# Optimization experiments

Hardware: AMD Instinct MI355X
Metric: run time of the kernel (lower is better)

Reference implementation:

```python
import jax, jax.numpy as jnp
import numpy as np

B, T, C = 4, 2048, 1024
H, DH = 16, 64  # num_heads, head_size; H*DH == C


def setup_inputs() -> dict:
    key = jax.random.key(0)
    ks = jax.random.split(key, 6)
    s = C ** -0.5  # mimic nn.Linear default init scale roughly
    x = jax.random.normal(ks[0], (B, T, C), dtype=jnp.float32)
    Wq = jax.random.normal(ks[1], (H, C, DH), dtype=jnp.float32) * s
    Wk = jax.random.normal(ks[2], (H, C, DH), dtype=jnp.float32) * s
    Wv = jax.random.normal(ks[3], (H, C, DH), dtype=jnp.float32) * s
    Wo = jax.random.normal(ks[4], (C, C), dtype=jnp.float32) * s
    bo = jax.random.normal(ks[5], (C,), dtype=jnp.float32) * s
    return {"x": x, "Wq": Wq, "Wk": Wk, "Wv": Wv, "Wo": Wo, "bo": bo}


def reference(x, Wq, Wk, Wv, Wo, bo):
    # per-head projections (no bias, as in nanoGPT Head)
    q = jnp.einsum('btc,hcd->bhtd', x, Wq)
    k = jnp.einsum('btc,hcd->bhtd', x, Wk)
    v = jnp.einsum('btc,hcd->bhtd', x, Wv)
    scale = DH ** -0.5
    scores = jnp.einsum('bhtd,bhsd->bhts', q, k) * scale  # [B,H,T,T]
    causal = jnp.tril(jnp.ones((T, T), dtype=bool))
    scores = jnp.where(causal, scores, jnp.float32(-jnp.inf))
    attn = jax.nn.softmax(scores, axis=-1)
    out = jnp.einsum('bhts,bhsd->bhtd', attn, v)  # [B,H,T,DH]
    out = out.transpose(0, 2, 1, 3).reshape(B, T, C)  # concat heads
    return out @ Wo.T + bo  # output projection (dropout=0.0 -> identity)
```

## Files before the change

### kernel.cpp

```cpp
#include <hip/hip_runtime.h>
#include <hip/hip_bf16.h>

constexpr int kB = 4, kT = 2048, kC = 1024, kH = 16, kD = 64;

typedef __attribute__((ext_vector_type(8))) short bf16x8;
typedef __attribute__((ext_vector_type(4))) short bf16x4;
typedef __attribute__((ext_vector_type(4))) float f32x4;
typedef unsigned short u16;

__device__ inline u16 f2b(float f) {
    __bf16 h = (__bf16)f;
    return __builtin_bit_cast(u16, h);
}

__device__ __forceinline__ void gl_lds16(const u16* g, u16* l) {
    __builtin_amdgcn_global_load_lds(
        (__attribute__((address_space(1))) const void*)g,
        (__attribute__((address_space(3))) void*)l, 16, 0, 0);
}

__global__ __launch_bounds__(256) void prep_kernel(const float* __restrict__ xf,
                                                   u16* __restrict__ xb,
                                                   const float* __restrict__ Wq,
                                                   const float* __restrict__ Wk,
                                                   const float* __restrict__ Wv,
                                                   u16* __restrict__ Wt) {
    __shared__ u16 tile[64][66];
    if (blockIdx.x < 8192) {
        int i = (blockIdx.x * 256 + threadIdx.x) * 4;
        float4 v = *(const float4*)(xf + i);
        ushort4 o;
        o.x = f2b(v.x); o.y = f2b(v.y); o.z = f2b(v.z); o.w = f2b(v.w);
        *(ushort4*)(xb + i) = o;
        return;
    }
    int blk = blockIdx.x - 8192;
    int ct = blk & 15;
    int h  = (blk >> 4) & 15;
    int which = blk >> 8;
    const float* W = (which == 0) ? Wq : (which == 1) ? Wk : Wv;
    const float* src = W + ((size_t)h * kC + ct * 64) * kD;
    int tid = threadIdx.x;
    int dr = (tid & 15) * 4;
    int cr = tid >> 4;
    #pragma unroll
    for (int pass = 0; pass < 4; pass++) {
        int c = pass * 16 + cr;
        float4 v = *(const float4*)(src + (size_t)c * kD + dr);
        tile[c][dr + 0] = f2b(v.x);
        tile[c][dr + 1] = f2b(v.y);
        tile[c][dr + 2] = f2b(v.z);
        tile[c][dr + 3] = f2b(v.w);
    }
    __syncthreads();
    u16* dst = Wt + ((size_t)(which * kH + h) * kD) * kC + ct * 64;
    int c4 = (tid & 15) * 4;
    int d0 = tid >> 4;
    #pragma unroll
    for (int pass = 0; pass < 4; pass++) {
        int d = pass * 16 + d0;
        ushort4 pk;
        pk.x = tile[c4 + 0][d];
        pk.y = tile[c4 + 1][d];
        pk.z = tile[c4 + 2][d];
        pk.w = tile[c4 + 3][d];
        *(ushort4*)(dst + (size_t)d * kC + c4) = pk;
    }
}

__global__ __launch_bounds__(256) void qkv_kernel(const u16* __restrict__ x,
                                                  const u16* __restrict__ Wt,
                                                  u16* __restrict__ q,
                                                  u16* __restrict__ k,
                                                  u16* __restrict__ vT) {
    __shared__ u16 Ash[128 * 32];
    __shared__ u16 Bsh[128 * 32];
    const int tid = threadIdx.x;
    const int lane = tid & 63;
    const int w = tid >> 6;
    const int mblk = blockIdx.x & 63;
    const int nblk = blockIdx.x >> 6;
    const int m0 = mblk * 128, n0 = nblk * 128;
    const int wm = (w >> 1) * 64, wn = (w & 1) * 64;
    const int col = lane & 15, quad = lane >> 4;

    const int rowa = tid >> 2;
    const int kc = (tid & 3) * 8;
    const u16* gA = x + (size_t)(m0 + rowa) * kC + kc;
    const u16* gB = Wt + (size_t)(n0 + rowa) * kC + kc;
    u16* lA = Ash + tid * 8;
    u16* lB = Bsh + tid * 8;

    f32x4 z = {0.f, 0.f, 0.f, 0.f};
    f32x4 acc[4][4];
    #pragma unroll
    for (int mi = 0; mi < 4; mi++)
        #pragma unroll
        for (int ni = 0; ni < 4; ni++) acc[mi][ni] = z;

    for (int k0 = 0; k0 < kC; k0 += 32) {
        __syncthreads();
        gl_lds16(gA + k0, lA);
        gl_lds16(gA + (size_t)64 * kC + k0, lA + 64 * 32);
        gl_lds16(gB + k0, lB);
        gl_lds16(gB + (size_t)64 * kC + k0, lB + 64 * 32);
        __syncthreads();
        bf16x8 a[4], b[4];
        #pragma unroll
        for (int mi = 0; mi < 4; mi++)
            a[mi] = *(const bf16x8*)&Ash[(wm + mi * 16 + col) * 32 + quad * 8];
        #pragma unroll
        for (int ni = 0; ni < 4; ni++)
            b[ni] = *(const bf16x8*)&Bsh[(wn + ni * 16 + col) * 32 + quad * 8];
        #pragma unroll
        for (int mi = 0; mi < 4; mi++)
            #pragma unroll
            for (int ni = 0; ni < 4; ni++)
                acc[mi][ni] = __builtin_amdgcn_mfma_f32_16x16x32_bf16(a[mi], b[ni], acc[mi][ni], 0, 0, 0);
    }

    const int nq = n0 + wn;
    const int which = nq >> 10;
    const int h = (nq & 1023) >> 6;
    const int mq = m0 + wm;
    const int b_ = mq >> 11;
    const int tq = mq & 2047;
    if (which < 2) {
        const float qs = (which == 0) ? 0.1803368801111204f : 1.0f;
        u16* base = ((which == 0) ? q : k) + ((size_t)(b_ * kH + h) * kT) * kD;
        #pragma unroll
        for (int mi = 0; mi < 4; mi++)
            #pragma unroll
            for (int ni = 0; ni < 4; ni++)
                #pragma unroll
                for (int r = 0; r < 4; r++) {
                    int t = tq + mi * 16 + quad * 4 + r;
                    base[(size_t)t * kD + ni * 16 + col] = f2b(acc[mi][ni][r] * qs);
                }
    } else {
        u16* base = vT + ((size_t)(b_ * kH + h) * kD) * kT;
        #pragma unroll
        for (int mi = 0; mi < 4; mi++)
            #pragma unroll
            for (int ni = 0; ni < 4; ni++) {
                int d = ni * 16 + col;
                int t = tq + mi * 16 + quad * 4;
                ushort4 pk;
                pk.x = f2b(acc[mi][ni][0]);
                pk.y = f2b(acc[mi][ni][1]);
                pk.z = f2b(acc[mi][ni][2]);
                pk.w = f2b(acc[mi][ni][3]);
                *(ushort4*)(base + (size_t)d * kT + t) = pk;
            }
    }
}

__device__ __forceinline__ void attn_step(const bf16x8 (&ka)[2][2],
                                          const bf16x4 (&va)[2][4],
                                          const bf16x8 (&qa)[2][2],
                                          f32x4 (&o)[2][4],
                                          float (&l_)[2],
                                          bool needmask,
                                          int s0, int t0, int col, int quad) {
    f32x4 z = {0.f, 0.f, 0.f, 0.f};
    f32x4 st[2][2];
    #pragma unroll
    for (int si = 0; si < 2; si++)
        #pragma unroll
        for (int mi = 0; mi < 2; mi++) {
            f32x4 a = __builtin_amdgcn_mfma_f32_16x16x32_bf16(ka[si][0], qa[mi][0], z, 0, 0, 0);
            st[si][mi] = __builtin_amdgcn_mfma_f32_16x16x32_bf16(ka[si][1], qa[mi][1], a, 0, 0, 0);
        }
    bf16x4 pb[2][2];
    #pragma unroll
    for (int mi = 0; mi < 2; mi++)
        #pragma unroll
        for (int si = 0; si < 2; si++) {
            bf16x4 pk;
            #pragma unroll
            for (int r = 0; r < 4; r++) {
                float p = __builtin_amdgcn_exp2f(st[si][mi][r]);
                if (needmask) {
                    int sg = s0 + si * 16 + quad * 4 + r;
                    int tg = t0 + mi * 16 + col;
                    if (sg > tg) p = 0.f;
                }
                l_[mi] += p;
                pk[r] = (short)f2b(p);
            }
            pb[mi][si] = pk;
        }
    #pragma unroll
    for (int si = 0; si < 2; si++)
        #pragma unroll
        for (int dt = 0; dt < 4; dt++)
            #pragma unroll
            for (int mi = 0; mi < 2; mi++)
                o[mi][dt] = __builtin_amdgcn_mfma_f32_16x16x16bf16_1k(va[si][dt], pb[mi][si], o[mi][dt], 0, 0, 0);
}

__global__ __launch_bounds__(256) void attn_kernel(const u16* __restrict__ q,
                                                   const u16* __restrict__ kmat,
                                                   const u16* __restrict__ vT,
                                                   u16* __restrict__ att,
                                                   const float* __restrict__ Wo,
                                                   u16* __restrict__ Wob) {
    __shared__ u16 shmem[4][2][4096];
    if (blockIdx.x >= 512) {
        int i = ((blockIdx.x - 512) * 256 + threadIdx.x) * 4;
        float4 v = *(const float4*)(Wo + i);
        ushort4 o;
        o.x = f2b(v.x); o.y = f2b(v.y); o.z = f2b(v.z); o.w = f2b(v.w);
        *(ushort4*)(Wob + i) = o;
        return;
    }
    const int tid = threadIdx.x;
    const int lane = tid & 63;
    const int w = tid >> 6;
    const int bh = blockIdx.x & 63;
    const int p8 = blockIdx.x >> 6;
    const int p = p8 * 4 + w;
    const int t0a = p * 32;
    const int t0b = (63 - p) * 32;
    const int Lw = 63 - p8 * 4 - w;
    const int col = lane & 15, quad = lane >> 4;

    const u16* qbase = q + (size_t)bh * kT * kD;
    const u16* kbase = kmat + (size_t)bh * kT * kD;
    const u16* vbase = vT + (size_t)bh * kD * kT;

    const u16* gK0 = kbase + (size_t)(lane >> 3) * kD + (((lane & 7) ^ (lane >> 3)) * 8);
    const u16* gV0 = vbase + (size_t)(lane >> 2) * kT + (((lane & 3) ^ ((lane >> 3) & 3)) * 8);

    bf16x8 qa[2][2][2];
    #pragma unroll
    for (int tile = 0; tile < 2; tile++) {
        int t0 = tile ? t0b : t0a;
        #pragma unroll
        for (int mi = 0; mi < 2; mi++)
            #pragma unroll
            for (int c2 = 0; c2 < 2; c2++)
                qa[tile][mi][c2] = *(const bf16x8*)(qbase + (size_t)(t0 + mi * 16 + col) * kD + c2 * 32 + quad * 8);
    }
    asm volatile("s_waitcnt vmcnt(0)" ::: "memory");

    f32x4 z = {0.f, 0.f, 0.f, 0.f};
    f32x4 oA[2][4], oB[2][4];
    #pragma unroll
    for (int mi = 0; mi < 2; mi++)
        #pragma unroll
        for (int dt = 0; dt < 4; dt++) { oA[mi][dt] = z; oB[mi][dt] = z; }
    float lA[2] = {0.f, 0.f}, lB[2] = {0.f, 0.f};

    auto stage = [&](int buf, int tile) {
        u16* Kd = &shmem[w][buf][0] + lane * 8;
        u16* Vd = &shmem[w][buf][2048] + lane * 8;
        const u16* gk = gK0 + (size_t)(tile * 32) * kD;
        const u16* gv = gV0 + tile * 32;
        #pragma unroll
        for (int i = 0; i < 4; i++) {
            gl_lds16(gk + (size_t)(i * 8) * kD, Kd + i * 512);
            gl_lds16(gv + (size_t)(i * 16) * kT, Vd + i * 512);
        }
    };

    stage(0, 0);
    if (Lw >= 1) stage(1, 1);
    for (int j = 0; j <= Lw; j++) {
        if (j < Lw) { asm volatile("s_waitcnt vmcnt(8)" ::: "memory"); }
        else        { asm volatile("s_waitcnt vmcnt(0)" ::: "memory"); }
        const int buf = j & 1;
        const u16* Kb = &shmem[w][buf][0];
        const u16* Vb = Kb + 2048;
        bf16x8 ka[2][2];
        #pragma unroll
        for (int si = 0; si < 2; si++) {
            int row = si * 16 + col;
            #pragma unroll
            for (int c2 = 0; c2 < 2; c2++)
                ka[si][c2] = *(const bf16x8*)&Kb[row * 64 + (((c2 * 4 + quad) ^ (row & 7)) * 8)];
        }
        bf16x4 va[2][4];
        #pragma unroll
        for (int si = 0; si < 2; si++)
            #pragma unroll
            for (int dt = 0; dt < 4; dt++) {
                int row = dt * 16 + col;
                int sb = si * 2 + (quad >> 1);
                va[si][dt] = *(const bf16x4*)&Vb[row * 32 + ((sb ^ ((row >> 1) & 3)) * 8) + (quad & 1) * 4];
            }
        asm volatile("s_waitcnt lgkmcnt(0)" ::: "memory");
        if (j + 2 <= Lw) stage(buf, j + 2);
        const int s0 = j * 32;
        attn_step(ka, va, qa[1], oB, lB, j == Lw, s0, t0b, col, quad);
        if (j <= p)
            attn_step(ka, va, qa[0], oA, lA, j == p, s0, t0a, col, quad);
    }

    #pragma unroll
    for (int mi = 0; mi < 2; mi++) {
        lA[mi] += __shfl_xor(lA[mi], 16, 64);
        lA[mi] += __shfl_xor(lA[mi], 32, 64);
        lB[mi] += __shfl_xor(lB[mi], 16, 64);
        lB[mi] += __shfl_xor(lB[mi], 32, 64);
    }

    const int b = bh / kH, hh = bh % kH;
    #pragma unroll
    for (int tile = 0; tile < 2; tile++) {
        int t0 = tile ? t0b : t0a;
        #pragma unroll
        for (int mi = 0; mi < 2; mi++) {
            float inv = 1.0f / (tile ? lB[mi] : lA[mi]);
            int t = t0 + mi * 16 + col;
            #pragma unroll
            for (int dt = 0; dt < 4; dt++) {
                f32x4 s = tile ? oB[mi][dt] : oA[mi][dt];
                ushort4 pk;
                pk.x = f2b(s[0] * inv);
                pk.y = f2b(s[1] * inv);
                pk.z = f2b(s[2] * inv);
                pk.w = f2b(s[3] * inv);
                *(ushort4*)(att + ((size_t)b * kT + t) * kC + hh * kD + dt * 16 + quad * 4) = pk;
            }
        }
    }
}

__global__ __launch_bounds__(256) void oproj_kernel(const u16* __restrict__ att,
                                                    const u16* __restrict__ Wo,
                                                    const float* __restrict__ bo,
                                                    float* __restrict__ out) {
    __shared__ u16 Ash[128 * 32];
    __shared__ u16 Bsh[128 * 32];
    const int tid = threadIdx.x;
    const int lane = tid & 63;
    const int w = tid >> 6;
    const int mblk = blockIdx.x & 63;
    const int nblk = blockIdx.x >> 6;
    const int m0 = mblk * 128, n0 = nblk * 128;
    const int wm = (w >> 1) * 64, wn = (w & 1) * 64;
    const int col = lane & 15, quad = lane >> 4;

    const int rowa = tid >> 2;
    const int kc = (tid & 3) * 8;
    const u16* gA = att + (size_t)(m0 + rowa) * kC + kc;
    const u16* gB = Wo + (size_t)(n0 + rowa) * kC + kc;
    u16* lA = Ash + tid * 8;
    u16* lB = Bsh + tid * 8;

    f32x4 z = {0.f, 0.f, 0.f, 0.f};
    f32x4 acc[4][4];
    #pragma unroll
    for (int mi = 0; mi < 4; mi++)
        #pragma unroll
        for (int ni = 0; ni < 4; ni++) acc[mi][ni] = z;

    for (int k0 = 0; k0 < kC; k0 += 32) {
        __syncthreads();
        gl_lds16(gA + k0, lA);
        gl_lds16(gA + (size_t)64 * kC + k0, lA + 64 * 32);
        gl_lds16(gB + k0, lB);
        gl_lds16(gB + (size_t)64 * kC + k0, lB + 64 * 32);
        __syncthreads();
        bf16x8 a[4], b[4];
        #pragma unroll
        for (int mi = 0; mi < 4; mi++)
            a[mi] = *(const bf16x8*)&Ash[(wm + mi * 16 + col) * 32 + quad * 8];
        #pragma unroll
        for (int ni = 0; ni < 4; ni++)
            b[ni] = *(const bf16x8*)&Bsh[(wn + ni * 16 + col) * 32 + quad * 8];
        #pragma unroll
        for (int mi = 0; mi < 4; mi++)
            #pragma unroll
            for (int ni = 0; ni < 4; ni++)
                acc[mi][ni] = __builtin_amdgcn_mfma_f32_16x16x32_bf16(a[mi], b[ni], acc[mi][ni], 0, 0, 0);
    }

    float bias[4];
    #pragma unroll
    for (int ni = 0; ni < 4; ni++) bias[ni] = bo[n0 + wn + ni * 16 + col];

    #pragma unroll
    for (int mi = 0; mi < 4; mi++)
        #pragma unroll
        for (int ni = 0; ni < 4; ni++)
            #pragma unroll
            for (int r = 0; r < 4; r++) {
                int m = m0 + wm + mi * 16 + quad * 4 + r;
                out[(size_t)m * kC + n0 + wn + ni * 16 + col] = acc[mi][ni][r] + bias[ni];
            }
}

extern "C" void kernel_launch(void* const* d_in, const int* in_sizes, int n_in,
                              void* d_out, int out_size, void* d_ws, size_t ws_size,
                              hipStream_t stream) {
    const float* x  = (const float*)d_in[0];
    const float* Wq = (const float*)d_in[1];
    const float* Wk = (const float*)d_in[2];
    const float* Wv = (const float*)d_in[3];
    const float* Wo = (const float*)d_in[4];
    const float* bo = (const float*)d_in[5];
    float* out = (float*)d_out;

    char* ws = (char*)d_ws;
    u16* Wt  = (u16*)ws;
    u16* xb  = Wt + (size_t)3 * kH * kD * kC;
    u16* qb  = xb + (size_t)kB * kT * kC;
    u16* kb  = qb + (size_t)kB * kH * kT * kD;
    u16* vTb = kb + (size_t)kB * kH * kT * kD;
    u16* att = xb;
    u16* Wob = Wt;

    prep_kernel<<<dim3(8192 + 768), dim3(256), 0, stream>>>(x, xb, Wq, Wk, Wv, Wt);
    qkv_kernel<<<dim3(1536), dim3(256), 0, stream>>>(xb, Wt, qb, kb, vTb);
    attn_kernel<<<dim3(512 + 1024), dim3(256), 0, stream>>>(qb, kb, vTb, att, Wo, Wob);
    oproj_kernel<<<dim3(512), dim3(256), 0, stream>>>(att, Wob, bo, out);
}
```

Baseline: 247.9 us.

## Rewrite QKV GEMM with 256x256 tiles, 4-stage LDS pipeline and swizzle

The QKV projection GEMM moves from 128x128 tiles with 256 threads and a single synchronous LDS buffer to 256x256 tiles with 512 threads. It uses a four-buffer global-to-LDS prefetch ring with explicit vmcnt waits, an XOR swizzle on LDS rows to avoid bank conflicts, and interleaved half-tile MFMA phases with s_setprio. The aim is to hide global load latency and raise data reuse per block. The cost is more registers, 128KB of LDS per block, and only 384 blocks, which may underfill the GPU.

```diff
diff --git a/kernel.cpp b/kernel.cpp
--- a/kernel.cpp
+++ b/kernel.cpp
@@ -68,55 +68,93 @@
     }
 }
 
-__global__ __launch_bounds__(256) void qkv_kernel(const u16* __restrict__ x,
-                                                  const u16* __restrict__ Wt,
-                                                  u16* __restrict__ q,
-                                                  u16* __restrict__ k,
-                                                  u16* __restrict__ vT) {
-    __shared__ u16 Ash[128 * 32];
-    __shared__ u16 Bsh[128 * 32];
+__global__ __launch_bounds__(512, 2) void qkv_kernel(const u16* __restrict__ x,
+                                                     const u16* __restrict__ Wt,
+                                                     u16* __restrict__ q,
+                                                     u16* __restrict__ k,
+                                                     u16* __restrict__ vT) {
+    __shared__ u16 lds[4][2][8192];
     const int tid = threadIdx.x;
     const int lane = tid & 63;
     const int w = tid >> 6;
-    const int mblk = blockIdx.x & 63;
-    const int nblk = blockIdx.x >> 6;
-    const int m0 = mblk * 128, n0 = nblk * 128;
-    const int wm = (w >> 1) * 64, wn = (w & 1) * 64;
+    const int mblk = blockIdx.x & 31;
+    const int nblk = blockIdx.x >> 5;
+    const int m0 = mblk * 256, n0 = nblk * 256;
+    const int wm = (w >> 2) * 128, wn = (w & 3) * 64;
     const int col = lane & 15, quad = lane >> 4;
 
-    const int rowa = tid >> 2;
-    const int kc = (tid & 3) * 8;
-    const u16* gA = x + (size_t)(m0 + rowa) * kC + kc;
-    const u16* gB = Wt + (size_t)(n0 + rowa) * kC + kc;
-    u16* lA = Ash + tid * 8;
-    u16* lB = Bsh + tid * 8;
+    const int r0 = tid >> 2, kp = tid & 3;
+    const int r1 = r0 + 128;
+    const u16* gA0 = x  + (size_t)(m0 + r0) * kC + ((kp ^ ((r0 >> 1) & 3)) * 8);
+    const u16* gA1 = x  + (size_t)(m0 + r1) * kC + ((kp ^ ((r1 >> 1) & 3)) * 8);
+    const u16* gB0 = Wt + (size_t)(n0 + r0) * kC + ((kp ^ ((r0 >> 1) & 3)) * 8);
+    const u16* gB1 = Wt + (size_t)(n0 + r1) * kC + ((kp ^ ((r1 >> 1) & 3)) * 8);
+
+    auto stageA = [&](int buf, int kt) {
+        gl_lds16(gA0 + kt * 32, &lds[buf][0][0] + tid * 8);
+        gl_lds16(gA1 + kt * 32, &lds[buf][0][0] + (512 + tid) * 8);
+    };
+    auto stageB = [&](int buf, int kt) {
+        gl_lds16(gB0 + kt * 32, &lds[buf][1][0] + tid * 8);
+        gl_lds16(gB1 + kt * 32, &lds[buf][1][0] + (512 + tid) * 8);
+    };
 
     f32x4 z = {0.f, 0.f, 0.f, 0.f};
-    f32x4 acc[4][4];
-    #pragma unroll
-    for (int mi = 0; mi < 4; mi++)
+    f32x4 acc[8][4];
+    #pragma unroll
+    for (int mi = 0; mi < 8; mi++)
         #pragma unroll
         for (int ni = 0; ni < 4; ni++) acc[mi][ni] = z;
 
-    for (int k0 = 0; k0 < kC; k0 += 32) {
-        __syncthreads();
-        gl_lds16(gA + k0, lA);
-        gl_lds16(gA + (size_t)64 * kC + k0, lA + 64 * 32);
-        gl_lds16(gB + k0, lB);
-        gl_lds16(gB + (size_t)64 * kC + k0, lB + 64 * 32);
-        __syncthreads();
-        bf16x8 a[4], b[4];
+    stageA(0, 0); stageB(0, 0);
+    stageA(1, 1); stageB(1, 1);
+    stageA(2, 2); stageB(2, 2);
+    asm volatile("s_waitcnt vmcnt(8)" ::: "memory");
+    __builtin_amdgcn_s_barrier();
+
+    for (int g = 0; g < 32; g++) {
+        const int buf = g & 3;
+        const int sb = (g + 3) & 3;
+        const bool dos = (g + 3) < 32;
+        bf16x8 b0[4], a0[4], a1[4];
+        #pragma unroll
+        for (int ni = 0; ni < 4; ni++) {
+            int row = wn + ni * 16 + col;
+            b0[ni] = *(const bf16x8*)&lds[buf][1][row * 32 + ((quad ^ ((row >> 1) & 3)) * 8)];
+        }
+        #pragma unroll
+        for (int mi = 0; mi < 4; mi++) {
+            int row = wm + mi * 16 + col;
+            a0[mi] = *(const bf16x8*)&lds[buf][0][row * 32 + ((quad ^ ((row >> 1) & 3)) * 8)];
+        }
+        if (dos) stageA(sb, g + 3);
+        __builtin_amdgcn_s_barrier();
+        __builtin_amdgcn_s_setprio(1);
         #pragma unroll
         for (int mi = 0; mi < 4; mi++)
-            a[mi] = *(const bf16x8*)&Ash[(wm + mi * 16 + col) * 32 + quad * 8];
-        #pragma unroll
-        for (int ni = 0; ni < 4; ni++)
-            b[ni] = *(const bf16x8*)&Bsh[(wn + ni * 16 + col) * 32 + quad * 8];
+            #pragma unroll
+            for (int ni = 0; ni < 4; ni++)
+                acc[mi][ni] = __builtin_amdgcn_mfma_f32_16x16x32_bf16(a0[mi], b0[ni], acc[mi][ni], 0, 0, 0);
+        __builtin_amdgcn_s_setprio(0);
+        __builtin_amdgcn_s_barrier();
+        #pragma unroll
+        for (int mi = 0; mi < 4; mi++) {
+            int row = wm + 64 + mi * 16 + col;
+            a1[mi] = *(const bf16x8*)&lds[buf][0][row * 32 + ((quad ^ ((row >> 1) & 3)) * 8)];
+        }
+        if (dos) stageB(sb, g + 3);
+        __builtin_amdgcn_s_barrier();
+        __builtin_amdgcn_s_setprio(1);
         #pragma unroll
         for (int mi = 0; mi < 4; mi++)
             #pragma unroll
             for (int ni = 0; ni < 4; ni++)
-                acc[mi][ni] = __builtin_amdgcn_mfma_f32_16x16x32_bf16(a[mi], b[ni], acc[mi][ni], 0, 0, 0);
+                acc[4 + mi][ni] = __builtin_amdgcn_mfma_f32_16x16x32_bf16(a1[mi], b0[ni], acc[4 + mi][ni], 0, 0, 0);
+        __builtin_amdgcn_s_setprio(0);
+        if (g < 29)       { asm volatile("s_waitcnt vmcnt(8)" ::: "memory"); }
+        else if (g == 29) { asm volatile("s_waitcnt vmcnt(4)" ::: "memory"); }
+        else if (g == 30) { asm volatile("s_waitcnt vmcnt(0)" ::: "memory"); }
+        __builtin_amdgcn_s_barrier();
     }
 
     const int nq = n0 + wn;
@@ -129,7 +167,7 @@
         const float qs = (which == 0) ? 0.1803368801111204f : 1.0f;
         u16* base = ((which == 0) ? q : k) + ((size_t)(b_ * kH + h) * kT) * kD;
         #pragma unroll
-        for (int mi = 0; mi < 4; mi++)
+        for (int mi = 0; mi < 8; mi++)
             #pragma unroll
             for (int ni = 0; ni < 4; ni++)
                 #pragma unroll
@@ -140,7 +178,7 @@
     } else {
         u16* base = vT + ((size_t)(b_ * kH + h) * kD) * kT;
         #pragma unroll
-        for (int mi = 0; mi < 4; mi++)
+        for (int mi = 0; mi < 8; mi++)
             #pragma unroll
             for (int ni = 0; ni < 4; ni++) {
                 int d = ni * 16 + col;
@@ -413,7 +451,7 @@
     u16* Wob = Wt;
 
     prep_kernel<<<dim3(8192 + 768), dim3(256), 0, stream>>>(x, xb, Wq, Wk, Wv, Wt);
-    qkv_kernel<<<dim3(1536), dim3(256), 0, stream>>>(xb, Wt, qb, kb, vTb);
+    qkv_kernel<<<dim3(384), dim3(512), 0, stream>>>(xb, Wt, qb, kb, vTb);
     attn_kernel<<<dim3(512 + 1024), dim3(256), 0, stream>>>(qb, kb, vTb, att, Wo, Wob);
     oproj_kernel<<<dim3(512), dim3(256), 0, stream>>>(att, Wob, bo, out);
 }
```

After: 250.7 us. Within noise of the previous version (+1.1%).

## Triple-buffer QKV GEMM LDS loads with swizzled layout and async waits

Applied to the files above, without the earlier changes.

Replaces the QKV projection GEMM's single-buffered LDS staging, which had two barriers per k-step, with a three-stage ring. Global-to-LDS loads for later k-tiles are issued while MFMA runs on the current tile, and manual vmcnt waits plus s_barrier control the handoff. It also XOR-swizzles the 8-element chunks within each 32-wide row to reduce LDS bank conflicts on the fragment reads. LDS use triples, and the hand-written waitcnt sequence is fragile: the compiler's own waits or a change in counts could break correctness.

```diff
diff --git a/kernel.cpp b/kernel.cpp
--- a/kernel.cpp
+++ b/kernel.cpp
@@ -73,8 +73,7 @@
                                                   u16* __restrict__ q,
                                                   u16* __restrict__ k,
                                                   u16* __restrict__ vT) {
-    __shared__ u16 Ash[128 * 32];
-    __shared__ u16 Bsh[128 * 32];
+    __shared__ u16 lds[3][2][4096];
     const int tid = threadIdx.x;
     const int lane = tid & 63;
     const int w = tid >> 6;
@@ -84,12 +83,19 @@
     const int wm = (w >> 1) * 64, wn = (w & 1) * 64;
     const int col = lane & 15, quad = lane >> 4;
 
-    const int rowa = tid >> 2;
-    const int kc = (tid & 3) * 8;
-    const u16* gA = x + (size_t)(m0 + rowa) * kC + kc;
-    const u16* gB = Wt + (size_t)(n0 + rowa) * kC + kc;
-    u16* lA = Ash + tid * 8;
-    u16* lB = Bsh + tid * 8;
+    const int r0 = tid >> 2, kp = tid & 3;
+    const int r1 = r0 + 64;
+    const u16* gA0 = x  + (size_t)(m0 + r0) * kC + ((kp ^ ((r0 >> 1) & 3)) * 8);
+    const u16* gA1 = x  + (size_t)(m0 + r1) * kC + ((kp ^ ((r1 >> 1) & 3)) * 8);
+    const u16* gB0 = Wt + (size_t)(n0 + r0) * kC + ((kp ^ ((r0 >> 1) & 3)) * 8);
+    const u16* gB1 = Wt + (size_t)(n0 + r1) * kC + ((kp ^ ((r1 >> 1) & 3)) * 8);
+
+    auto stage = [&](int buf, int kt) {
+        gl_lds16(gA0 + kt * 32, &lds[buf][0][0] + tid * 8);
+        gl_lds16(gA1 + kt * 32, &lds[buf][0][0] + (256 + tid) * 8);
+        gl_lds16(gB0 + kt * 32, &lds[buf][1][0] + tid * 8);
+        gl_lds16(gB1 + kt * 32, &lds[buf][1][0] + (256 + tid) * 8);
+    };
 
     f32x4 z = {0.f, 0.f, 0.f, 0.f};
     f32x4 acc[4][4];
@@ -98,26 +104,46 @@
         #pragma unroll
         for (int ni = 0; ni < 4; ni++) acc[mi][ni] = z;
 
-    for (int k0 = 0; k0 < kC; k0 += 32) {
-        __syncthreads();
-        gl_lds16(gA + k0, lA);
-        gl_lds16(gA + (size_t)64 * kC + k0, lA + 64 * 32);
-        gl_lds16(gB + k0, lB);
-        gl_lds16(gB + (size_t)64 * kC + k0, lB + 64 * 32);
-        __syncthreads();
+    auto body = [&](int j) {
+        const u16* A  = &lds[j % 3][0][0];
+        const u16* Bb = &lds[j % 3][1][0];
         bf16x8 a[4], b[4];
         #pragma unroll
-        for (int mi = 0; mi < 4; mi++)
-            a[mi] = *(const bf16x8*)&Ash[(wm + mi * 16 + col) * 32 + quad * 8];
-        #pragma unroll
-        for (int ni = 0; ni < 4; ni++)
-            b[ni] = *(const bf16x8*)&Bsh[(wn + ni * 16 + col) * 32 + quad * 8];
+        for (int mi = 0; mi < 4; mi++) {
+            int row = wm + mi * 16 + col;
+            a[mi] = *(const bf16x8*)&A[row * 32 + ((quad ^ ((row >> 1) & 3)) * 8)];
+        }
+        #pragma unroll
+        for (int ni = 0; ni < 4; ni++) {
+            int row = wn + ni * 16 + col;
+            b[ni] = *(const bf16x8*)&Bb[row * 32 + ((quad ^ ((row >> 1) & 3)) * 8)];
+        }
         #pragma unroll
         for (int mi = 0; mi < 4; mi++)
             #pragma unroll
             for (int ni = 0; ni < 4; ni++)
                 acc[mi][ni] = __builtin_amdgcn_mfma_f32_16x16x32_bf16(a[mi], b[ni], acc[mi][ni], 0, 0, 0);
-    }
+    };
+
+    stage(0, 0);
+    stage(1, 1);
+    stage(2, 2);
+    asm volatile("s_waitcnt vmcnt(8)" ::: "memory");
+    asm volatile("s_barrier" ::: "memory");
+
+    for (int j = 0; j < 29; j++) {
+        body(j);
+        asm volatile("s_waitcnt vmcnt(4)" ::: "memory");
+        asm volatile("s_barrier" ::: "memory");
+        stage(j % 3, j + 3);
+    }
+    body(29);
+    asm volatile("s_waitcnt vmcnt(4)" ::: "memory");
+    asm volatile("s_barrier" ::: "memory");
+    body(30);
+    asm volatile("s_waitcnt vmcnt(0)" ::: "memory");
+    asm volatile("s_barrier" ::: "memory");
+    body(31);
 
     const int nq = n0 + wn;
     const int which = nq >> 10;
```

After: 247.8 us. No clear change (-0.0%).
